# Optimization experiments

Hardware: AMD Instinct MI355X
Metric: run time of the kernel (lower is better)

Reference implementation:

```python
import jax, jax.numpy as jnp
import numpy as np

B, T, D = 2, 2048, 2048
Q_HEADS, KV_HEADS, HEAD_DIM = 16, 4, 128
ROPE_BASE = 10000.0


def _apply_rotary(x_nhd, positions_n):
    # x_nhd: (N, H, head_dim); half-split rotary embedding.
    half = x_nhd.shape[-1] // 2
    inv_freq = 1.0 / (ROPE_BASE ** (jnp.arange(half, dtype=jnp.float32) / half))
    ang = positions_n.astype(jnp.float32)[:, None] * inv_freq  # (N, half)
    cos = jnp.cos(ang)[:, None, :]  # (N, 1, half)
    sin = jnp.sin(ang)[:, None, :]
    x1, x2 = x_nhd[..., :half], x_nhd[..., half:]
    return jnp.concatenate([x1 * cos - x2 * sin, x1 * sin + x2 * cos], axis=-1)


def setup_inputs() -> dict:
    key = jax.random.key(0)
    ks = jax.random.split(key, 5)
    s_in = 1.0 / np.sqrt(D)
    s_o = 1.0 / np.sqrt(Q_HEADS * HEAD_DIM)
    x = jax.random.normal(ks[0], (B, T, D), dtype=jnp.float32)
    positions = jnp.broadcast_to(jnp.arange(T, dtype=jnp.int32), (B, T))
    wq = jax.random.normal(ks[1], (Q_HEADS * HEAD_DIM, D), dtype=jnp.float32) * s_in
    wk = jax.random.normal(ks[2], (KV_HEADS * HEAD_DIM, D), dtype=jnp.float32) * s_in
    wv = jax.random.normal(ks[3], (KV_HEADS * HEAD_DIM, D), dtype=jnp.float32) * s_in
    wo = jax.random.normal(ks[4], (D, Q_HEADS * HEAD_DIM), dtype=jnp.float32) * s_o
    return {"x": x, "positions": positions, "wq": wq, "wk": wk, "wv": wv, "wo": wo}


def reference(x, positions, wq, wk, wv, wo):
    bsz, tsz, _ = x.shape
    q = jnp.einsum('btd,od->bto', x, wq).reshape(bsz, tsz, Q_HEADS, HEAD_DIM)
    k = jnp.einsum('btd,od->bto', x, wk).reshape(bsz, tsz, KV_HEADS, HEAD_DIM)
    v = jnp.einsum('btd,od->bto', x, wv).reshape(bsz, tsz, KV_HEADS, HEAD_DIM)
    pos_flat = positions.reshape(-1)
    q = _apply_rotary(q.reshape(-1, Q_HEADS, HEAD_DIM), pos_flat).reshape(bsz, tsz, Q_HEADS, HEAD_DIM)
    k = _apply_rotary(k.reshape(-1, KV_HEADS, HEAD_DIM), pos_flat).reshape(bsz, tsz, KV_HEADS, HEAD_DIM)
    rep = Q_HEADS // KV_HEADS
    k = jnp.repeat(k, rep, axis=2)
    v = jnp.repeat(v, rep, axis=2)
    logits = jnp.einsum('bthd,bThd->bhtT', q, k) / jnp.sqrt(jnp.float32(HEAD_DIM))
    causal = jnp.tril(jnp.ones((tsz, tsz), dtype=bool))
    logits = jnp.where(causal[None, None], logits, -1e9)
    weights = jax.nn.softmax(logits, axis=-1)
    ctx = jnp.einsum('bhtT,bThd->bthd', weights, v).reshape(bsz, tsz, Q_HEADS * HEAD_DIM)
    return jnp.einsum('bto,do->btd', ctx, wo)
```

## Files before the change

### kernel.cpp

```cpp
#include <hip/hip_runtime.h>
#include <hip/hip_bf16.h>

typedef __bf16 bf16x8 __attribute__((ext_vector_type(8)));
typedef float  f32x4  __attribute__((ext_vector_type(4)));
typedef float  f32x16 __attribute__((ext_vector_type(16)));
typedef unsigned int u32x2 __attribute__((ext_vector_type(2)));

#define B_   2
#define T_   2048
#define D_   2048
#define QH_  16
#define KVH_ 4
#define HD_  128
#define BT_  (B_ * T_)
#define KVD_ 512
#define SCL  0.12751744f

#define GLOAD_LDS16(g, l)                                        \
  __builtin_amdgcn_global_load_lds(                              \
      (const __attribute__((address_space(1))) void*)(g),        \
      (__attribute__((address_space(3))) void*)(l), 16, 0, 0)

__global__ __launch_bounds__(256) void cvt_all(
    const float* __restrict__ x, const float* __restrict__ wq,
    const float* __restrict__ wk, const float* __restrict__ wv,
    const float* __restrict__ wo, ushort* __restrict__ out) {
  const int i = blockIdx.x * 256 + threadIdx.x;
  int j = i;
  const float* src;
  float mul = 1.f;
  if (j < 2097152) { src = x; }
  else if ((j -= 2097152) < 1048576) { src = wq; mul = SCL; }
  else if ((j -= 1048576) < 262144)  { src = wk; }
  else if ((j -= 262144) < 262144)   { src = wv; }
  else { j -= 262144; src = wo; }
  float4 v = ((const float4*)src)[j];
  __hip_bfloat16 h0 = __float2bfloat16(v.x * mul);
  __hip_bfloat16 h1 = __float2bfloat16(v.y * mul);
  __hip_bfloat16 h2 = __float2bfloat16(v.z * mul);
  __hip_bfloat16 h3 = __float2bfloat16(v.w * mul);
  ushort4 o;
  o.x = *(ushort*)&h0; o.y = *(ushort*)&h1;
  o.z = *(ushort*)&h2; o.w = *(ushort*)&h3;
  ((ushort4*)out)[i] = o;
}

__global__ __launch_bounds__(256) void gemm_qkv(
    const ushort* __restrict__ X, const ushort* __restrict__ WQ,
    const ushort* __restrict__ WK, const ushort* __restrict__ WV,
    ushort* __restrict__ qo, ushort* __restrict__ ko, ushort* __restrict__ vo) {
  const int nb = blockIdx.x % 24;
  const int mb = blockIdx.x / 24;
  const int tid = threadIdx.x;
  const int wave = tid >> 6;
  const int lane = tid & 63;
  const int mrow = lane & 15;
  const int quad = lane >> 4;
  const int wm = wave >> 1;
  const int wn = wave & 1;
  const int m0 = mb * 128;
  const int K = D_;

  const ushort* Wg;
  if (nb < 16)      Wg = WQ + (size_t)nb * 128 * K;
  else if (nb < 20) Wg = WK + (size_t)(nb - 16) * 128 * K;
  else              Wg = WV + (size_t)(nb - 20) * 128 * K;

  __shared__ __align__(16) ushort At[128 * 64];
  __shared__ __align__(16) ushort Bt[128 * 64];

  f32x4 acc[4][4];
#pragma unroll
  for (int i = 0; i < 4; ++i)
#pragma unroll
    for (int j = 0; j < 4; ++j) acc[i][j] = (f32x4){0.f, 0.f, 0.f, 0.f};

  const ushort* Xg = X + (size_t)m0 * K;

  for (int k0 = 0; k0 < K; k0 += 64) {
#pragma unroll
    for (int p = 0; p < 4; ++p) {
      const int c = p * 256 + tid;
      const int row = c >> 3;
      const int cc = (c & 7) ^ (row & 7);
      GLOAD_LDS16(Xg + (size_t)row * K + k0 + cc * 8,
                  At + (size_t)(p * 256 + wave * 64) * 8);
      GLOAD_LDS16(Wg + (size_t)row * K + k0 + cc * 8,
                  Bt + (size_t)(p * 256 + wave * 64) * 8);
    }
    __syncthreads();

#pragma unroll
    for (int s = 0; s < 2; ++s) {
      bf16x8 af[4], bfr[4];
#pragma unroll
      for (int mt = 0; mt < 4; ++mt) {
        const int row = wm * 64 + mt * 16 + mrow;
        af[mt] = *reinterpret_cast<const bf16x8*>(
            At + row * 64 + (((s * 4 + quad) ^ (row & 7)) * 8));
      }
#pragma unroll
      for (int nt = 0; nt < 4; ++nt) {
        const int row = wn * 64 + nt * 16 + mrow;
        bfr[nt] = *reinterpret_cast<const bf16x8*>(
            Bt + row * 64 + (((s * 4 + quad) ^ (row & 7)) * 8));
      }
#pragma unroll
      for (int mt = 0; mt < 4; ++mt)
#pragma unroll
        for (int nt = 0; nt < 4; ++nt)
          acc[mt][nt] = __builtin_amdgcn_mfma_f32_16x16x32_bf16(
              af[mt], bfr[nt], acc[mt][nt], 0, 0, 0);
    }
    __syncthreads();
  }

#pragma unroll
  for (int mt = 0; mt < 4; ++mt) {
#pragma unroll
    for (int nt = 0; nt < 4; ++nt) {
      const int colw = wn * 64 + nt * 16 + mrow;
      const int row0 = m0 + wm * 64 + mt * 16 + quad * 4;
      if (nb < 16) {
        const int col = nb * 128 + colw;
#pragma unroll
        for (int r = 0; r < 4; ++r) {
          __hip_bfloat16 hh = __float2bfloat16(acc[mt][nt][r]);
          qo[(size_t)(row0 + r) * 2048 + col] = *(ushort*)&hh;
        }
      } else if (nb < 20) {
        const int col = (nb - 16) * 128 + colw;
#pragma unroll
        for (int r = 0; r < 4; ++r) {
          __hip_bfloat16 hh = __float2bfloat16(acc[mt][nt][r]);
          ko[(size_t)(row0 + r) * KVD_ + col] = *(ushort*)&hh;
        }
      } else {
        const int col = (nb - 20) * 128 + colw;
        const int bb = row0 >> 11;
        const int t0 = row0 & (T_ - 1);
        ushort4 s4;
#pragma unroll
        for (int r = 0; r < 4; ++r) {
          __hip_bfloat16 hh = __float2bfloat16(acc[mt][nt][r]);
          (&s4.x)[r] = *(ushort*)&hh;
        }
        *(ushort4*)(vo + ((size_t)(bb * KVD_ + col)) * T_ + t0) = s4;
      }
    }
  }
}

__global__ __launch_bounds__(256) void gemm_o(
    const ushort* __restrict__ X, const ushort* __restrict__ W,
    float* __restrict__ Y, int M, int N, int K) {
  const int nb128 = N >> 7;
  const int mb = blockIdx.x / nb128;
  const int nb = blockIdx.x % nb128;
  const int tid = threadIdx.x;
  const int wave = tid >> 6;
  const int lane = tid & 63;
  const int mrow = lane & 15;
  const int quad = lane >> 4;
  const int wm = wave >> 1;
  const int wn = wave & 1;
  const int m0 = mb * 128;
  const int n0 = nb * 128;

  __shared__ __align__(16) ushort At[128 * 64];
  __shared__ __align__(16) ushort Bt[128 * 64];

  f32x4 acc[4][4];
#pragma unroll
  for (int i = 0; i < 4; ++i)
#pragma unroll
    for (int j = 0; j < 4; ++j) acc[i][j] = (f32x4){0.f, 0.f, 0.f, 0.f};

  const ushort* Xg = X + (size_t)m0 * K;
  const ushort* Wg = W + (size_t)n0 * K;

  for (int k0 = 0; k0 < K; k0 += 64) {
#pragma unroll
    for (int p = 0; p < 4; ++p) {
      const int c = p * 256 + tid;
      const int row = c >> 3;
      const int cc = (c & 7) ^ (row & 7);
      GLOAD_LDS16(Xg + (size_t)row * K + k0 + cc * 8,
                  At + (size_t)(p * 256 + wave * 64) * 8);
      GLOAD_LDS16(Wg + (size_t)row * K + k0 + cc * 8,
                  Bt + (size_t)(p * 256 + wave * 64) * 8);
    }
    __syncthreads();

#pragma unroll
    for (int s = 0; s < 2; ++s) {
      bf16x8 af[4], bfr[4];
#pragma unroll
      for (int mt = 0; mt < 4; ++mt) {
        const int row = wm * 64 + mt * 16 + mrow;
        af[mt] = *reinterpret_cast<const bf16x8*>(
            At + row * 64 + (((s * 4 + quad) ^ (row & 7)) * 8));
      }
#pragma unroll
      for (int nt = 0; nt < 4; ++nt) {
        const int row = wn * 64 + nt * 16 + mrow;
        bfr[nt] = *reinterpret_cast<const bf16x8*>(
            Bt + row * 64 + (((s * 4 + quad) ^ (row & 7)) * 8));
      }
#pragma unroll
      for (int mt = 0; mt < 4; ++mt)
#pragma unroll
        for (int nt = 0; nt < 4; ++nt)
          acc[mt][nt] = __builtin_amdgcn_mfma_f32_16x16x32_bf16(
              af[mt], bfr[nt], acc[mt][nt], 0, 0, 0);
    }
    __syncthreads();
  }

#pragma unroll
  for (int mt = 0; mt < 4; ++mt)
#pragma unroll
    for (int nt = 0; nt < 4; ++nt) {
      const int col = n0 + wn * 64 + nt * 16 + mrow;
      const int row0 = m0 + wm * 64 + mt * 16 + quad * 4;
#pragma unroll
      for (int r = 0; r < 4; ++r)
        Y[(size_t)(row0 + r) * N + col] = acc[mt][nt][r];
    }
}

__global__ __launch_bounds__(256) void rope_kernel(
    __hip_bfloat16* __restrict__ q, __hip_bfloat16* __restrict__ k,
    const int* __restrict__ positions) {
  const int wave = threadIdx.x >> 6;
  const int lane = threadIdx.x & 63;
  const int p = blockIdx.x * 4 + wave;
  const int head = p % (QH_ + KVH_);
  const int bt = p / (QH_ + KVH_);

  __hip_bfloat16* base;
  if (head < QH_) base = q + ((size_t)bt * QH_ + head) * HD_;
  else            base = k + ((size_t)bt * KVH_ + (head - QH_)) * HD_;

  const float pos = (float)positions[bt];
  const float inv_freq = exp2f((float)lane * -0.20762050593f);
  const float ang = pos * inv_freq;
  const float c = cosf(ang);
  const float s = sinf(ang);

  const float x1 = __bfloat162float(base[lane]);
  const float x2 = __bfloat162float(base[lane + 64]);
  base[lane]      = __float2bfloat16(x1 * c - x2 * s);
  base[lane + 64] = __float2bfloat16(x1 * s + x2 * c);
}

static __device__ __forceinline__ unsigned pk2(float a, float b) {
  __hip_bfloat16 ha = __float2bfloat16(a);
  __hip_bfloat16 hb = __float2bfloat16(b);
  return (unsigned)(*(ushort*)&ha) | ((unsigned)(*(ushort*)&hb) << 16);
}

static __device__ __forceinline__ void hswap(unsigned& a, unsigned& b,
                                             const int hi) {
#if __has_builtin(__builtin_amdgcn_permlane32_swap)
  u32x2 r = __builtin_amdgcn_permlane32_swap(a, b, false, false);
  a = r.x;
  b = r.y;
#else
  unsigned s = __shfl_xor(hi ? a : b, 32, 64);
  unsigned na = hi ? s : a;
  b = hi ? b : s;
  a = na;
#endif
}

__global__ __launch_bounds__(256, 2) void attn_mfma(
    const ushort* __restrict__ q, const ushort* __restrict__ k,
    const ushort* __restrict__ vt, ushort* __restrict__ ctx) {
  const int tid = threadIdx.x;
  const int wave = tid >> 6;
  const int lane = tid & 63;
  const int m5 = lane & 31;
  const int hi = lane >> 5;

  int i = blockIdx.x;
  int bh, qt;
  if (i < 256) { bh = i >> 5; qt = 63 - (i & 31); }
  else { i -= 256; bh = i >> 5; qt = i & 31; }
  const int hkv = bh & 3;
  const int b   = bh >> 2;
  const int h   = hkv * 4 + wave;
  const int q0  = qt * 32;

  __shared__ __align__(16) ushort kt[2][64 * 128];
  __shared__ __align__(16) ushort vtile[2][128 * 64];

  const ushort* qrow =
      q + ((size_t)(b * T_ + q0 + m5) * QH_ + h) * HD_ + hi * 8;
  bf16x8 qf[8];
#pragma unroll
  for (int c = 0; c < 8; ++c)
    qf[c] = *reinterpret_cast<const bf16x8*>(qrow + c * 16);

  f32x16 o4[4];
#pragma unroll
  for (int dt = 0; dt < 4; ++dt)
#pragma unroll
    for (int r = 0; r < 16; ++r) o4[dt][r] = 0.f;
  float ls = 0.f;

  const ushort* kbase = k + ((size_t)b * T_ * KVH_ + hkv) * HD_;
  const ushort* vbase = vt + (size_t)(b * KVD_ + hkv * HD_) * T_;

  const int nblk = (q0 + 32 + 63) >> 6;

#pragma unroll
  for (int p = 0; p < 4; ++p) {
    const int c = p * 256 + tid;
    const int krow = c >> 4;
    const int kco = (c & 15) ^ (krow & 15);
    GLOAD_LDS16(kbase + (size_t)krow * KVD_ + kco * 8,
                kt[0] + (size_t)(p * 256 + wave * 64) * 8);
    const int vrow = c >> 3;
    const int vco = (c & 7) ^ (vrow & 7);
    GLOAD_LDS16(vbase + (size_t)vrow * T_ + vco * 8,
                vtile[0] + (size_t)(p * 256 + wave * 64) * 8);
  }
  __syncthreads();

  for (int blk = 0; blk < nblk; ++blk) {
    const int cur = blk & 1;
    const int j0 = blk * 64;

    if (blk + 1 < nblk) {
      const int j1 = j0 + 64;
#pragma unroll
      for (int p = 0; p < 4; ++p) {
        const int c = p * 256 + tid;
        const int krow = c >> 4;
        const int kco = (c & 15) ^ (krow & 15);
        GLOAD_LDS16(kbase + (size_t)(j1 + krow) * KVD_ + kco * 8,
                    kt[cur ^ 1] + (size_t)(p * 256 + wave * 64) * 8);
        const int vrow = c >> 3;
        const int vco = (c & 7) ^ (vrow & 7);
        GLOAD_LDS16(vbase + (size_t)vrow * T_ + j1 + vco * 8,
                    vtile[cur ^ 1] + (size_t)(p * 256 + wave * 64) * 8);
      }
    }

    const ushort* pk_ = kt[cur];
    const ushort* pv = vtile[cur];

#pragma unroll
    for (int t2 = 0; t2 < 2; ++t2) {
      f32x16 sa0, sa1;
#pragma unroll
      for (int r = 0; r < 16; ++r) { sa0[r] = 0.f; sa1[r] = 0.f; }
      const int rowk = t2 * 32 + m5;
#pragma unroll
      for (int c = 0; c < 8; c += 2) {
        const int ch0 = (2 * c + hi) ^ (rowk & 15);
        bf16x8 kf0 =
            *reinterpret_cast<const bf16x8*>(pk_ + rowk * 128 + ch0 * 8);
        sa0 = __builtin_amdgcn_mfma_f32_32x32x16_bf16(kf0, qf[c], sa0, 0, 0, 0);
        const int ch1 = (2 * (c + 1) + hi) ^ (rowk & 15);
        bf16x8 kf1 =
            *reinterpret_cast<const bf16x8*>(pk_ + rowk * 128 + ch1 * 8);
        sa1 = __builtin_amdgcn_mfma_f32_32x32x16_bf16(kf1, qf[c + 1], sa1,
                                                      0, 0, 0);
      }
      f32x16 sa = sa0 + sa1;

      float p[16];
      if (blk == nblk - 1) {
#pragma unroll
        for (int r = 0; r < 16; ++r) {
          const int key = j0 + t2 * 32 + (r & 3) + 8 * (r >> 2) + 4 * hi;
          p[r] = (key > q0 + m5) ? 0.f : exp2f(sa[r]);
        }
      } else {
#pragma unroll
        for (int r = 0; r < 16; ++r) p[r] = exp2f(sa[r]);
      }
#pragma unroll
      for (int r = 0; r < 16; ++r) ls += p[r];

      unsigned u0 = pk2(p[0], p[1]),   u1 = pk2(p[2], p[3]);
      unsigned u2 = pk2(p[4], p[5]),   u3 = pk2(p[6], p[7]);
      unsigned u4 = pk2(p[8], p[9]),   u5 = pk2(p[10], p[11]);
      unsigned u6 = pk2(p[12], p[13]), u7 = pk2(p[14], p[15]);
      hswap(u0, u2, hi); hswap(u1, u3, hi);
      hswap(u4, u6, hi); hswap(u5, u7, hi);

#pragma unroll
      for (int half = 0; half < 2; ++half) {
        union { unsigned w[4]; bf16x8 v; } pa;
        pa.w[0] = half ? u4 : u0;
        pa.w[1] = half ? u5 : u1;
        pa.w[2] = half ? u6 : u2;
        pa.w[3] = half ? u7 : u3;
        const int c = t2 * 2 + half;
#pragma unroll
        for (int dt = 0; dt < 4; ++dt) {
          const int rowv = dt * 32 + m5;
          const int chv = (2 * c + hi) ^ (rowv & 7);
          bf16x8 vf =
              *reinterpret_cast<const bf16x8*>(pv + rowv * 64 + chv * 8);
          o4[dt] =
              __builtin_amdgcn_mfma_f32_32x32x16_bf16(pa.v, vf, o4[dt], 0, 0, 0);
        }
      }
    }

    __syncthreads();
  }

  const float lt = ls + __shfl_xor(ls, 32, 64);
#pragma unroll
  for (int reg = 0; reg < 16; ++reg) {
    const int qrw = (reg & 3) + 8 * (reg >> 2) + 4 * hi;
    const float rl = 1.f / __shfl(lt, qrw, 64);
    ushort* op =
        ctx + ((size_t)(b * T_ + q0 + qrw) * QH_ + h) * HD_ + m5;
#pragma unroll
    for (int dt = 0; dt < 4; ++dt) {
      __hip_bfloat16 hb = __float2bfloat16(o4[dt][reg] * rl);
      op[dt * 32] = *(ushort*)&hb;
    }
  }
}

extern "C" void kernel_launch(void* const* d_in, const int* in_sizes, int n_in,
                              void* d_out, int out_size, void* d_ws, size_t ws_size,
                              hipStream_t stream) {
  const float* x  = (const float*)d_in[0];
  const int* pos  = (const int*)d_in[1];
  const float* wq = (const float*)d_in[2];
  const float* wk = (const float*)d_in[3];
  const float* wv = (const float*)d_in[4];
  const float* wo = (const float*)d_in[5];

  ushort* xb  = (ushort*)d_ws;
  ushort* wqb = xb  + (size_t)8388608;
  ushort* wkb = wqb + (size_t)4194304;
  ushort* wvb = wkb + (size_t)1048576;
  ushort* wob = wvb + (size_t)1048576;
  ushort* qb  = wob + (size_t)4194304;
  ushort* kb  = qb  + (size_t)8388608;
  ushort* vtb = kb  + (size_t)2097152;
  ushort* ctx = xb;

  cvt_all<<<18432, 256, 0, stream>>>(x, wq, wk, wv, wo, (ushort*)d_ws);

  gemm_qkv<<<(BT_ / 128) * 24, 256, 0, stream>>>(xb, wqb, wkb, wvb, qb, kb, vtb);

  rope_kernel<<<(BT_ * (QH_ + KVH_)) / 4, 256, 0, stream>>>(
      (__hip_bfloat16*)qb, (__hip_bfloat16*)kb, pos);

  attn_mfma<<<512, 256, 0, stream>>>(qb, kb, vtb, ctx);

  gemm_o<<<(BT_ / 128) * (D_ / 128), 256, 0, stream>>>(
      ctx, wob, (float*)d_out, BT_, D_, QH_ * HD_);
}
```

Before: 326.2 us.

## Double-buffer LDS tiles in QKV and output projection GEMMs

Both projection GEMMs now use two LDS buffers per operand and prefetch the K-tile two steps ahead with direct global-to-LDS loads. Partial vmcnt waits let the next tile's loads stay in flight while the current tile is consumed by MFMAs, which should hide global memory latency. The cost is twice the shared memory per block, which may lower occupancy. Correctness rests on the hand-written waitcnt/barrier sequence.

```diff
diff --git a/kernel.cpp b/kernel.cpp
--- a/kernel.cpp
+++ b/kernel.cpp
@@ -66,8 +66,8 @@
   else if (nb < 20) Wg = WK + (size_t)(nb - 16) * 128 * K;
   else              Wg = WV + (size_t)(nb - 20) * 128 * K;
 
-  __shared__ __align__(16) ushort At[128 * 64];
-  __shared__ __align__(16) ushort Bt[128 * 64];
+  __shared__ __align__(16) ushort At[2][128 * 64];
+  __shared__ __align__(16) ushort Bt[2][128 * 64];
 
   f32x4 acc[4][4];
 #pragma unroll
@@ -77,19 +77,31 @@
 
   const ushort* Xg = X + (size_t)m0 * K;
 
-  for (int k0 = 0; k0 < K; k0 += 64) {
+  auto STAGE = [&](int buf, int k0) {
 #pragma unroll
     for (int p = 0; p < 4; ++p) {
       const int c = p * 256 + tid;
       const int row = c >> 3;
       const int cc = (c & 7) ^ (row & 7);
       GLOAD_LDS16(Xg + (size_t)row * K + k0 + cc * 8,
-                  At + (size_t)(p * 256 + wave * 64) * 8);
+                  At[buf] + (size_t)(p * 256 + wave * 64) * 8);
       GLOAD_LDS16(Wg + (size_t)row * K + k0 + cc * 8,
-                  Bt + (size_t)(p * 256 + wave * 64) * 8);
-    }
-    __syncthreads();
-
+                  Bt[buf] + (size_t)(p * 256 + wave * 64) * 8);
+    }
+  };
+
+  const int NT = K / 64;
+  STAGE(0, 0);
+  STAGE(1, 64);
+
+  for (int t = 0; t < NT; ++t) {
+    const int cur = t & 1;
+    if (t + 2 < NT) asm volatile("s_waitcnt vmcnt(8)" ::: "memory");
+    else            asm volatile("s_waitcnt vmcnt(0)" ::: "memory");
+    __builtin_amdgcn_s_barrier();
+
+    const ushort* Ac = At[cur];
+    const ushort* Bc = Bt[cur];
 #pragma unroll
     for (int s = 0; s < 2; ++s) {
       bf16x8 af[4], bfr[4];
@@ -97,13 +109,13 @@
       for (int mt = 0; mt < 4; ++mt) {
         const int row = wm * 64 + mt * 16 + mrow;
         af[mt] = *reinterpret_cast<const bf16x8*>(
-            At + row * 64 + (((s * 4 + quad) ^ (row & 7)) * 8));
+            Ac + row * 64 + (((s * 4 + quad) ^ (row & 7)) * 8));
       }
 #pragma unroll
       for (int nt = 0; nt < 4; ++nt) {
         const int row = wn * 64 + nt * 16 + mrow;
         bfr[nt] = *reinterpret_cast<const bf16x8*>(
-            Bt + row * 64 + (((s * 4 + quad) ^ (row & 7)) * 8));
+            Bc + row * 64 + (((s * 4 + quad) ^ (row & 7)) * 8));
       }
 #pragma unroll
       for (int mt = 0; mt < 4; ++mt)
@@ -112,7 +124,10 @@
           acc[mt][nt] = __builtin_amdgcn_mfma_f32_16x16x32_bf16(
               af[mt], bfr[nt], acc[mt][nt], 0, 0, 0);
     }
-    __syncthreads();
+
+    asm volatile("s_waitcnt lgkmcnt(0)" ::: "memory");
+    __builtin_amdgcn_s_barrier();
+    if (t + 2 < NT) STAGE(cur, (t + 2) * 64);
   }
 
 #pragma unroll
@@ -167,8 +182,8 @@
   const int m0 = mb * 128;
   const int n0 = nb * 128;
 
-  __shared__ __align__(16) ushort At[128 * 64];
-  __shared__ __align__(16) ushort Bt[128 * 64];
+  __shared__ __align__(16) ushort At[2][128 * 64];
+  __shared__ __align__(16) ushort Bt[2][128 * 64];
 
   f32x4 acc[4][4];
 #pragma unroll
@@ -179,19 +194,31 @@
   const ushort* Xg = X + (size_t)m0 * K;
   const ushort* Wg = W + (size_t)n0 * K;
 
-  for (int k0 = 0; k0 < K; k0 += 64) {
+  auto STAGE = [&](int buf, int k0) {
 #pragma unroll
     for (int p = 0; p < 4; ++p) {
       const int c = p * 256 + tid;
       const int row = c >> 3;
       const int cc = (c & 7) ^ (row & 7);
       GLOAD_LDS16(Xg + (size_t)row * K + k0 + cc * 8,
-                  At + (size_t)(p * 256 + wave * 64) * 8);
+                  At[buf] + (size_t)(p * 256 + wave * 64) * 8);
       GLOAD_LDS16(Wg + (size_t)row * K + k0 + cc * 8,
-                  Bt + (size_t)(p * 256 + wave * 64) * 8);
-    }
-    __syncthreads();
-
+                  Bt[buf] + (size_t)(p * 256 + wave * 64) * 8);
+    }
+  };
+
+  const int NT = K / 64;
+  STAGE(0, 0);
+  STAGE(1, 64);
+
+  for (int t = 0; t < NT; ++t) {
+    const int cur = t & 1;
+    if (t + 2 < NT) asm volatile("s_waitcnt vmcnt(8)" ::: "memory");
+    else            asm volatile("s_waitcnt vmcnt(0)" ::: "memory");
+    __builtin_amdgcn_s_barrier();
+
+    const ushort* Ac = At[cur];
+    const ushort* Bc = Bt[cur];
 #pragma unroll
     for (int s = 0; s < 2; ++s) {
       bf16x8 af[4], bfr[4];
@@ -199,13 +226,13 @@
       for (int mt = 0; mt < 4; ++mt) {
         const int row = wm * 64 + mt * 16 + mrow;
         af[mt] = *reinterpret_cast<const bf16x8*>(
-            At + row * 64 + (((s * 4 + quad) ^ (row & 7)) * 8));
+            Ac + row * 64 + (((s * 4 + quad) ^ (row & 7)) * 8));
       }
 #pragma unroll
       for (int nt = 0; nt < 4; ++nt) {
         const int row = wn * 64 + nt * 16 + mrow;
         bfr[nt] = *reinterpret_cast<const bf16x8*>(
-            Bt + row * 64 + (((s * 4 + quad) ^ (row & 7)) * 8));
+            Bc + row * 64 + (((s * 4 + quad) ^ (row & 7)) * 8));
       }
 #pragma unroll
       for (int mt = 0; mt < 4; ++mt)
@@ -214,7 +241,10 @@
           acc[mt][nt] = __builtin_amdgcn_mfma_f32_16x16x32_bf16(
               af[mt], bfr[nt], acc[mt][nt], 0, 0, 0);
     }
-    __syncthreads();
+
+    asm volatile("s_waitcnt lgkmcnt(0)" ::: "memory");
+    __builtin_amdgcn_s_barrier();
+    if (t + 2 < NT) STAGE(cur, (t + 2) * 64);
   }
 
 #pragma unroll
```

Result: faster. 313.0 us (-4.1%).
